# Kernel optimization log

Hardware: AMD Instinct MI355X
Metric: run time of the kernel (lower is better)

The kernel has to match this reference:

```python
import jax, jax.numpy as jnp
import numpy as np

FACTOR = 5  # init factor


def setup_inputs() -> dict:
    key = jax.random.key(0)
    k1, k2, k3, k4 = jax.random.split(key, 4)
    B, H, L, D = 4, 8, 2048, 64
    sample_k = min(FACTOR * int(np.ceil(np.log(L))), L)  # 40
    queries = jax.random.normal(k1, (B, H, L, D), dtype=jnp.float32)
    keys = jax.random.normal(k2, (B, H, L, D), dtype=jnp.float32)
    values = jax.random.normal(k3, (B, H, L, D), dtype=jnp.float32)
    index_sample = jax.random.randint(k4, (L, sample_k), 0, L)
    return {"queries": queries, "keys": keys, "values": values,
            "index_sample": index_sample}


def reference(queries, keys, values, index_sample):
    B, H, L_Q, D = queries.shape
    L_K = keys.shape[2]
    n_top = min(FACTOR * int(np.ceil(np.log(L_Q))), L_Q)

    # --- _prob_QK ---
    # Gather sampled keys per query position: [B,H,L_Q,sample_k,D]
    K_sample = keys[:, :, index_sample, :]
    # Q.unsqueeze(3) @ K_sample^T -> [B,H,L_Q,sample_k]
    Q_K_sample = jnp.einsum('bhld,bhlsd->bhls', queries, K_sample)
    # sparsity measure M = max - mean
    M = Q_K_sample.max(axis=-1) - Q_K_sample.sum(axis=-1) / L_K
    _, M_top = jax.lax.top_k(M, n_top)  # [B,H,n_top]
    # gather top queries: [B,H,n_top,D]
    Q_reduce = jnp.take_along_axis(queries, M_top[..., None], axis=2)
    # full scores for top queries: [B,H,n_top,L_K]
    scores_top = jnp.einsum('bhud,bhkd->bhuk', Q_reduce, keys)

    # --- scale ---
    scale = 1.0 / np.sqrt(D).astype(np.float32)
    scores_top = scores_top * scale

    # --- initial context (mask_flag=False): mean of V broadcast over L_Q ---
    V_mean = values.mean(axis=2)  # [B,H,D]
    context = jnp.broadcast_to(V_mean[:, :, None, :], (B, H, L_Q, D))

    # --- update context at top-query positions ---
    attn = jax.nn.softmax(scores_top, axis=-1)           # [B,H,n_top,L_K]
    ctx_update = jnp.einsum('bhuk,bhkd->bhud', attn, values)
    b_idx = jnp.arange(B)[:, None, None]
    h_idx = jnp.arange(H)[None, :, None]
    context = context.at[b_idx, h_idx, M_top].set(ctx_update)
    return context
```

## Files before the change

### kernel.cpp

```cpp
#include <hip/hip_runtime.h>
#include <math.h>

#define BH 32
#define L  2048
#define D  64
#define SK 40
#define NT 40
#define NC 32
#define CK 64
#define SP 65
#define SCALE 0.125f

#define WS_M      0
#define WS_MTOP   262144
#define WS_VP     267264
#define WS_VM     529408
#define WS_QTOP   537600
#define WS_OPART  865280
#define WS_MPART  11351040
#define WS_LPART  11514880

template <int CTRL>
__device__ __forceinline__ float dpp_add(float x) {
    int y = __builtin_amdgcn_update_dpp(0, __float_as_int(x), CTRL, 0xF, 0xF, true);
    return x + __int_as_float(y);
}

__global__ __launch_bounds__(512) void kMV(const float* __restrict__ Q,
                                           const float* __restrict__ K,
                                           const float* __restrict__ V,
                                           const int* __restrict__ idx,
                                           float* __restrict__ M,
                                           float* __restrict__ Vp)
{
    __shared__ int   sidx[64 * SK];
    __shared__ float red[512];

    int t    = threadIdx.x;
    int b    = blockIdx.x;
    int head = ((b >> 3) & 3) * 8 + (b & 7);
    int qc   = b >> 5;
    int l0   = qc * 64;

    {
        int d = t & 63, r = t >> 6;
        const float* Vb = V + ((size_t)head * L + l0 + r * 8) * D + d;
        float acc = 0.f;
        #pragma unroll
        for (int k = 0; k < 8; ++k) acc += Vb[(size_t)k * D];
        red[t] = acc;
    }
    for (int i = t; i < 64 * SK; i += 512) sidx[i] = idx[l0 * SK + i];
    __syncthreads();
    if (t < 64) {
        float s = 0.f;
        #pragma unroll
        for (int rr = 0; rr < 8; ++rr) s += red[t + rr * 64];
        Vp[(head * 32 + qc) * 64 + t] = s;
    }

    int wave = t >> 6, lane = t & 63;
    int g16  = lane >> 4;
    int dl   = lane & 15;

    const float4* Q4  = reinterpret_cast<const float4*>(Q);
    const float4* Kb4 = reinterpret_cast<const float4*>(K) + (size_t)head * L * 16;

    #pragma unroll
    for (int qr = 0; qr < 2; ++qr) {
        int lq = wave * 8 + qr * 4 + g16;
        size_t qid = (size_t)head * L + (l0 + lq);
        float4 q4 = Q4[qid * 16 + dl];

        float mx = -INFINITY, sm = 0.f;
        #pragma unroll 4
        for (int s = 0; s < SK; ++s) {
            int kr = sidx[lq * SK + s];
            float4 k4 = Kb4[(size_t)kr * 16 + dl];
            float p = q4.x * k4.x + q4.y * k4.y + q4.z * k4.z + q4.w * k4.w;
            p = dpp_add<0xB1>(p);
            p = dpp_add<0x4E>(p);
            p = dpp_add<0x12C>(p);
            p = dpp_add<0x128>(p);
            mx = fmaxf(mx, p);
            sm += p;
        }
        if (dl == 0) M[qid] = mx - sm * (1.0f / (float)L);
    }
}

__global__ __launch_bounds__(256) void kTopVm(const float* __restrict__ M,
                                              const float* __restrict__ Vp,
                                              const float* __restrict__ Q,
                                              int* __restrict__ Mtop,
                                              float* __restrict__ Vm,
                                              float* __restrict__ Qtop)
{
    __shared__ unsigned int keys[L];
    __shared__ int hist[256];
    __shared__ int wtot[4];
    __shared__ unsigned int pref_s;
    __shared__ int krem_s;
    __shared__ int cnt_gt, cnt_eq;
    __shared__ int eqlist[64];
    __shared__ int stop[NT];

    int bh = blockIdx.x;
    int t  = threadIdx.x;
    int lane = t & 63, w = t >> 6;

    if (t < 64) {
        float s = 0.f;
        #pragma unroll
        for (int c = 0; c < 32; ++c) s += Vp[(bh * 32 + c) * 64 + t];
        Vm[bh * D + t] = s * (1.0f / (float)L);
    }

    for (int i = t; i < L; i += 256) {
        unsigned int u = __float_as_uint(M[bh * L + i]);
        keys[i] = (u & 0x80000000u) ? ~u : (u | 0x80000000u);
    }
    if (t == 0) { pref_s = 0u; krem_s = NT; cnt_gt = 0; cnt_eq = 0; }
    __syncthreads();

    #pragma unroll
    for (int shift = 24; shift >= 0; shift -= 8) {
        hist[t] = 0;
        __syncthreads();
        unsigned int pref = pref_s;
        int krem = krem_s;
        for (int i = t; i < L; i += 256) {
            unsigned int k  = keys[i];
            unsigned int hi = (shift == 24) ? 0u : (k >> (shift + 8));
            if (hi == pref) atomicAdd(&hist[(k >> shift) & 0xFF], 1);
        }
        __syncthreads();
        int h = hist[t];
        int v = h;
        #pragma unroll
        for (int o = 1; o < 64; o <<= 1) {
            int u = __shfl_down(v, o, 64);
            if (lane + o < 64) v += u;
        }
        if (lane == 0) wtot[w] = v;
        __syncthreads();
        int ss = v;
        #pragma unroll
        for (int w2 = 1; w2 < 4; ++w2) if (w2 > w) ss += wtot[w2];
        if (ss - h < krem && ss >= krem) {
            krem_s = krem - (ss - h);
            pref_s = (pref << 8) | (unsigned int)t;
        }
    }
    __syncthreads();

    unsigned int T = pref_s;
    int krem = krem_s;
    for (int i = t; i < L; i += 256) {
        unsigned int k = keys[i];
        if (k > T) {
            int p = atomicAdd(&cnt_gt, 1);
            Mtop[bh * NT + p] = i;
            stop[p] = i;
        } else if (k == T) {
            int p = atomicAdd(&cnt_eq, 1);
            if (p < 64) eqlist[p] = i;
        }
    }
    __syncthreads();
    if (t == 0) {
        int base = cnt_gt;
        int m = cnt_eq < 64 ? cnt_eq : 64;
        for (int q = 0; q < krem; ++q) {
            int best = 0x7fffffff, bj = -1;
            for (int j = 0; j < m; ++j) if (eqlist[j] < best) { best = eqlist[j]; bj = j; }
            Mtop[bh * NT + base + q] = best;
            stop[base + q] = best;
            if (bj >= 0) eqlist[bj] = 0x7fffffff;
        }
    }
    __syncthreads();
    const float4* Qg = reinterpret_cast<const float4*>(Q) + (size_t)bh * L * 16;
    float4* Qt = reinterpret_cast<float4*>(Qtop) + (size_t)bh * NT * 16;
    for (int i = t; i < NT * 16; i += 256)
        Qt[i] = Qg[(size_t)stop[i >> 4] * 16 + (i & 15)];
}

__global__ __launch_bounds__(256) void kAttnPart(const float* __restrict__ Qtop,
                                                 const float* __restrict__ K,
                                                 const float* __restrict__ V,
                                                 const float* __restrict__ Vm,
                                                 float* __restrict__ Opart,
                                                 float* __restrict__ mpart,
                                                 float* __restrict__ lpart,
                                                 float* __restrict__ out)
{
    __shared__ float4 V4s[CK * 16];
    __shared__ float  S[NT * SP];
    __shared__ float  smax[NT], ssum[NT];

    int c = blockIdx.x, bh = blockIdx.y;
    int t = threadIdx.x;

    {
        const float4* Vm4 = reinterpret_cast<const float4*>(Vm + bh * D);
        float4* outB = reinterpret_cast<float4*>(out) + ((size_t)bh * L + c * CK) * 16;
        #pragma unroll
        for (int k = 0; k < 4; ++k) { int i = t + k * 256; outB[i] = Vm4[i & 15]; }
    }

    const float4* Vg = reinterpret_cast<const float4*>(V) + ((size_t)bh * L + c * CK) * 16;
    float4 vreg[4];
    #pragma unroll
    for (int k = 0; k < 4; ++k) vreg[k] = Vg[t + k * 256];

    int w    = __builtin_amdgcn_readfirstlane(t) >> 6;
    int lane = t & 63;
    const float4* Kg = reinterpret_cast<const float4*>(K) + ((size_t)bh * L + c * CK) * 16;
    float4 k[16];
    #pragma unroll
    for (int d4 = 0; d4 < 16; ++d4) k[d4] = Kg[(size_t)lane * 16 + d4];

    const float4* Qb = reinterpret_cast<const float4*>(Qtop) + ((size_t)bh * NT + w * 10) * 16;
    float p[10];
    #pragma unroll
    for (int i = 0; i < 10; ++i) {
        float a0 = 0.f;
        #pragma unroll
        for (int d4 = 0; d4 < 16; ++d4) {
            float4 q4 = Qb[i * 16 + d4];
            a0 += q4.x * k[d4].x + q4.y * k[d4].y + q4.z * k[d4].z + q4.w * k[d4].w;
        }
        p[i] = a0 * SCALE;
    }

    #pragma unroll
    for (int i = 0; i < 10; ++i) {
        int u = w * 10 + i;
        float m = p[i];
        #pragma unroll
        for (int o = 1; o < 64; o <<= 1) m = fmaxf(m, __shfl_xor(m, o, 64));
        float e = __expf(p[i] - m);
        float l2 = e;
        #pragma unroll
        for (int o = 1; o < 64; o <<= 1) l2 += __shfl_xor(l2, o, 64);
        S[u * SP + lane] = e;
        if (lane == 0) { smax[u] = m; ssum[u] = l2; }
    }

    #pragma unroll
    for (int kk = 0; kk < 4; ++kk) {
        int i = t + kk * 256;
        int j = i >> 4, d4 = i & 15;
        V4s[j * 16 + (d4 ^ (j & 15))] = vreg[kk];
    }
    __syncthreads();

    {
        int a = t >> 5, r = t & 31;
        int d4 = r >> 1, jh = r & 1;
        float4 acc[5];
        #pragma unroll
        for (int ui = 0; ui < 5; ++ui) acc[ui] = make_float4(0.f, 0.f, 0.f, 0.f);
        for (int jj = 0; jj < 32; ++jj) {
            int j = jh * 32 + jj;
            float4 v4 = V4s[j * 16 + (d4 ^ (j & 15))];
            #pragma unroll
            for (int ui = 0; ui < 5; ++ui) {
                float pw = S[(a + 8 * ui) * SP + j];
                acc[ui].x += pw * v4.x; acc[ui].y += pw * v4.y;
                acc[ui].z += pw * v4.z; acc[ui].w += pw * v4.w;
            }
        }
        #pragma unroll
        for (int ui = 0; ui < 5; ++ui) {
            acc[ui].x = dpp_add<0xB1>(acc[ui].x);
            acc[ui].y = dpp_add<0xB1>(acc[ui].y);
            acc[ui].z = dpp_add<0xB1>(acc[ui].z);
            acc[ui].w = dpp_add<0xB1>(acc[ui].w);
        }
        if (jh == 0) {
            float4* Og = reinterpret_cast<float4*>(Opart) + ((size_t)(bh * NC + c) * NT) * 16;
            #pragma unroll
            for (int ui = 0; ui < 5; ++ui)
                Og[(a + 8 * ui) * 16 + d4] = acc[ui];
        }
    }
    if (t < NT) {
        mpart[(bh * NC + c) * NT + t] = smax[t];
        lpart[(bh * NC + c) * NT + t] = ssum[t];
    }
}

__global__ __launch_bounds__(64) void kCombine(const float* __restrict__ Opart,
                                               const float* __restrict__ mpart,
                                               const float* __restrict__ lpart,
                                               const int* __restrict__ Mtop,
                                               float* __restrict__ out)
{
    int u = blockIdx.x, bh = blockIdx.y, d = threadIdx.x;
    float gm = -INFINITY;
    #pragma unroll
    for (int c = 0; c < NC; ++c) gm = fmaxf(gm, mpart[(bh * NC + c) * NT + u]);
    float den = 0.f, o = 0.f;
    #pragma unroll
    for (int c = 0; c < NC; ++c) {
        int pi = (bh * NC + c) * NT + u;
        float wgt = __expf(mpart[pi] - gm);
        den += wgt * lpart[pi];
        o   += wgt * Opart[(size_t)pi * D + d];
    }
    int qrow = Mtop[bh * NT + u];
    out[((size_t)bh * L + qrow) * D + d] = o / den;
}

extern "C" void kernel_launch(void* const* d_in, const int* in_sizes, int n_in,
                              void* d_out, int out_size, void* d_ws, size_t ws_size,
                              hipStream_t stream)
{
    const float* Q   = (const float*)d_in[0];
    const float* K   = (const float*)d_in[1];
    const float* V   = (const float*)d_in[2];
    const int*   idx = (const int*)d_in[3];
    float* out = (float*)d_out;

    char* ws = (char*)d_ws;
    float* M     = (float*)(ws + WS_M);
    int*   Mtop  = (int*)  (ws + WS_MTOP);
    float* Vp    = (float*)(ws + WS_VP);
    float* Vm    = (float*)(ws + WS_VM);
    float* Qtop  = (float*)(ws + WS_QTOP);
    float* Opart = (float*)(ws + WS_OPART);
    float* mpart = (float*)(ws + WS_MPART);
    float* lpart = (float*)(ws + WS_LPART);

    kMV      <<<1024, 512, 0, stream>>>(Q, K, V, idx, M, Vp);
    kTopVm   <<<BH, 256, 0, stream>>>(M, Vp, Q, Mtop, Vm, Qtop);
    kAttnPart<<<dim3(NC, BH), 256, 0, stream>>>(Qtop, K, V, Vm, Opart, mpart, lpart, out);
    kCombine <<<dim3(NT, BH), 64, 0, stream>>>(Opart, mpart, lpart, Mtop, out);
}
```

Baseline: 165.1 us.

## Halve attention key chunk size, split head dim across half-waves, dual accumulators in sampling

The attention-partial kernel now processes 32-key chunks over 64 chunks per head instead of 64-key chunks over 32. Each lane holds half of a key row's head dimension, and the two halves are summed with a cross-half shuffle. This doubles the grid and halves per-thread key registers, aiming for better occupancy and more parallel blocks, but doubles the partial outputs that the combine kernel must read and merge. The sampling kernel also splits max/sum into two accumulators with deeper unrolling to expose ILP.

```diff
diff --git a/kernel.cpp b/kernel.cpp
--- a/kernel.cpp
+++ b/kernel.cpp
@@ -6,9 +6,9 @@
 #define D  64
 #define SK 40
 #define NT 40
-#define NC 32
-#define CK 64
-#define SP 65
+#define NC 64
+#define CK 32
+#define SPB 33
 #define SCALE 0.125f
 
 #define WS_M      0
@@ -17,8 +17,8 @@
 #define WS_VM     529408
 #define WS_QTOP   537600
 #define WS_OPART  865280
-#define WS_MPART  11351040
-#define WS_LPART  11514880
+#define WS_MPART  21836800
+#define WS_LPART  22164480
 
 template <int CTRL>
 __device__ __forceinline__ float dpp_add(float x) {
@@ -72,8 +72,8 @@
         size_t qid = (size_t)head * L + (l0 + lq);
         float4 q4 = Q4[qid * 16 + dl];
 
-        float mx = -INFINITY, sm = 0.f;
-        #pragma unroll 4
+        float mx0 = -INFINITY, mx1 = -INFINITY, sm0 = 0.f, sm1 = 0.f;
+        #pragma unroll 8
         for (int s = 0; s < SK; ++s) {
             int kr = sidx[lq * SK + s];
             float4 k4 = Kb4[(size_t)kr * 16 + dl];
@@ -82,10 +82,10 @@
             p = dpp_add<0x4E>(p);
             p = dpp_add<0x12C>(p);
             p = dpp_add<0x128>(p);
-            mx = fmaxf(mx, p);
-            sm += p;
-        }
-        if (dl == 0) M[qid] = mx - sm * (1.0f / (float)L);
+            if (s & 1) { mx1 = fmaxf(mx1, p); sm1 += p; }
+            else       { mx0 = fmaxf(mx0, p); sm0 += p; }
+        }
+        if (dl == 0) M[qid] = fmaxf(mx0, mx1) - (sm0 + sm1) * (1.0f / (float)L);
     }
 }
 
@@ -196,7 +196,7 @@
                                                  float* __restrict__ out)
 {
     __shared__ float4 V4s[CK * 16];
-    __shared__ float  S[NT * SP];
+    __shared__ float  S[NT * SPB];
     __shared__ float  smax[NT], ssum[NT];
 
     int c = blockIdx.x, bh = blockIdx.y;
@@ -206,20 +206,17 @@
         const float4* Vm4 = reinterpret_cast<const float4*>(Vm + bh * D);
         float4* outB = reinterpret_cast<float4*>(out) + ((size_t)bh * L + c * CK) * 16;
         #pragma unroll
-        for (int k = 0; k < 4; ++k) { int i = t + k * 256; outB[i] = Vm4[i & 15]; }
-    }
-
-    const float4* Vg = reinterpret_cast<const float4*>(V) + ((size_t)bh * L + c * CK) * 16;
-    float4 vreg[4];
-    #pragma unroll
-    for (int k = 0; k < 4; ++k) vreg[k] = Vg[t + k * 256];
+        for (int k = 0; k < 2; ++k) { int i = t + k * 256; outB[i] = Vm4[i & 15]; }
+    }
 
     int w    = __builtin_amdgcn_readfirstlane(t) >> 6;
     int lane = t & 63;
+    int row  = lane & 31;
+    int dh   = (lane >> 5) * 8;
     const float4* Kg = reinterpret_cast<const float4*>(K) + ((size_t)bh * L + c * CK) * 16;
-    float4 k[16];
-    #pragma unroll
-    for (int d4 = 0; d4 < 16; ++d4) k[d4] = Kg[(size_t)lane * 16 + d4];
+    float4 k[8];
+    #pragma unroll
+    for (int d4 = 0; d4 < 8; ++d4) k[d4] = Kg[row * 16 + dh + d4];
 
     const float4* Qb = reinterpret_cast<const float4*>(Qtop) + ((size_t)bh * NT + w * 10) * 16;
     float p[10];
@@ -227,10 +224,11 @@
     for (int i = 0; i < 10; ++i) {
         float a0 = 0.f;
         #pragma unroll
-        for (int d4 = 0; d4 < 16; ++d4) {
-            float4 q4 = Qb[i * 16 + d4];
+        for (int d4 = 0; d4 < 8; ++d4) {
+            float4 q4 = Qb[i * 16 + dh + d4];
             a0 += q4.x * k[d4].x + q4.y * k[d4].y + q4.z * k[d4].z + q4.w * k[d4].w;
         }
+        a0 += __shfl_xor(a0, 32, 64);
         p[i] = a0 * SCALE;
     }
 
@@ -239,20 +237,23 @@
         int u = w * 10 + i;
         float m = p[i];
         #pragma unroll
-        for (int o = 1; o < 64; o <<= 1) m = fmaxf(m, __shfl_xor(m, o, 64));
+        for (int o = 1; o < 32; o <<= 1) m = fmaxf(m, __shfl_xor(m, o, 64));
         float e = __expf(p[i] - m);
         float l2 = e;
         #pragma unroll
-        for (int o = 1; o < 64; o <<= 1) l2 += __shfl_xor(l2, o, 64);
-        S[u * SP + lane] = e;
+        for (int o = 1; o < 32; o <<= 1) l2 += __shfl_xor(l2, o, 64);
+        if (lane < 32) S[u * SPB + row] = e;
         if (lane == 0) { smax[u] = m; ssum[u] = l2; }
     }
 
-    #pragma unroll
-    for (int kk = 0; kk < 4; ++kk) {
-        int i = t + kk * 256;
-        int j = i >> 4, d4 = i & 15;
-        V4s[j * 16 + (d4 ^ (j & 15))] = vreg[kk];
+    {
+        const float4* Vg = reinterpret_cast<const float4*>(V) + ((size_t)bh * L + c * CK) * 16;
+        float4 v0 = Vg[t];
+        float4 v1 = Vg[t + 256];
+        int i0 = t,       j0 = i0 >> 4, c0 = i0 & 15;
+        int i1 = t + 256, j1 = i1 >> 4, c1 = i1 & 15;
+        V4s[j0 * 16 + (c0 ^ (j0 & 15))] = v0;
+        V4s[j1 * 16 + (c1 ^ (j1 & 15))] = v1;
     }
     __syncthreads();
 
@@ -262,12 +263,12 @@
         float4 acc[5];
         #pragma unroll
         for (int ui = 0; ui < 5; ++ui) acc[ui] = make_float4(0.f, 0.f, 0.f, 0.f);
-        for (int jj = 0; jj < 32; ++jj) {
-            int j = jh * 32 + jj;
+        for (int jj = 0; jj < 16; ++jj) {
+            int j = jh * 16 + jj;
             float4 v4 = V4s[j * 16 + (d4 ^ (j & 15))];
             #pragma unroll
             for (int ui = 0; ui < 5; ++ui) {
-                float pw = S[(a + 8 * ui) * SP + j];
+                float pw = S[(a + 8 * ui) * SPB + j];
                 acc[ui].x += pw * v4.x; acc[ui].y += pw * v4.y;
                 acc[ui].z += pw * v4.z; acc[ui].w += pw * v4.w;
             }
@@ -300,10 +301,10 @@
 {
     int u = blockIdx.x, bh = blockIdx.y, d = threadIdx.x;
     float gm = -INFINITY;
-    #pragma unroll
+    #pragma unroll 8
     for (int c = 0; c < NC; ++c) gm = fmaxf(gm, mpart[(bh * NC + c) * NT + u]);
     float den = 0.f, o = 0.f;
-    #pragma unroll
+    #pragma unroll 8
     for (int c = 0; c < NC; ++c) {
         int pi = (bh * NC + c) * NT + u;
         float wgt = __expf(mpart[pi] - gm);
```

Measured after the change: 191.0 us. +15.7%, slower.
